# Kernel tuning notes

Measured on AMD Instinct MI355X. Metric: run time of the kernel, lower is better.

## Reference

```python
import jax, jax.numpy as jnp
import numpy as np

B, T, I, H, O = 512, 512, 128, 50, 10


def setup_inputs() -> dict:
    key = jax.random.key(0)
    ks = jax.random.split(key, 7)
    return {
        "x": jax.random.normal(ks[0], (B, T, I), dtype=jnp.float32),
        "W_ih": jax.random.normal(ks[1], (4 * H, I), dtype=jnp.float32) * 0.05,
        "W_hh": jax.random.normal(ks[2], (4 * H, H), dtype=jnp.float32) * 0.05,
        "b_ih": jax.random.normal(ks[3], (4 * H,), dtype=jnp.float32) * 0.05,
        "b_hh": jax.random.normal(ks[4], (4 * H,), dtype=jnp.float32) * 0.05,
        "W_fc": jax.random.normal(ks[5], (O, H), dtype=jnp.float32) * 0.05,
        "b_fc": jax.random.normal(ks[6], (O,), dtype=jnp.float32) * 0.05,
    }


def reference(x, W_ih, W_hh, b_ih, b_hh, W_fc, b_fc):
    # Single-layer LSTM (PyTorch gate order i,f,g,o), batch_first, zero init state.
    Bsz = x.shape[0]
    Hd = W_hh.shape[1]
    bias = b_ih + b_hh  # [4H]
    # Precompute input projections for all timesteps: [T, B, 4H]
    x_proj = jnp.einsum('bti,gi->tbg', x, W_ih) + bias

    def step(carry, xp_t):
        h, c = carry  # [B, H] each
        gates = xp_t + h @ W_hh.T  # [B, 4H]
        i, f, g, o = jnp.split(gates, 4, axis=-1)
        i = jax.nn.sigmoid(i)
        f = jax.nn.sigmoid(f)
        g = jnp.tanh(g)
        o = jax.nn.sigmoid(o)
        c = f * c + i * g
        h = o * jnp.tanh(c)
        return (h, c), None

    h0 = jnp.zeros((Bsz, Hd), dtype=x.dtype)
    c0 = jnp.zeros((Bsz, Hd), dtype=x.dtype)
    (h_last, _), _ = jax.lax.scan(step, (h0, c0), x_proj)
    return h_last @ W_fc.T + b_fc  # [B, O]
```

## Files before the change

### kernel.cpp

```cpp
#include <hip/hip_runtime.h>


#define BB 512
#define TT 512
#define II 128
#define HH 50
#define GG 200

typedef _Float16 half2v __attribute__((ext_vector_type(2)));
typedef _Float16 half8v __attribute__((ext_vector_type(8)));
typedef float float4v __attribute__((ext_vector_type(4)));

#if defined(__has_builtin)
#if __has_builtin(__builtin_amdgcn_fdot2)
#define HAVE_FDOT2 1
#endif
#if __has_builtin(__builtin_amdgcn_rcpf)
#define HAVE_RCPF 1
#endif
#endif

__device__ __forceinline__ float fdot2f(half2v a, half2v b, float c) {
#ifdef HAVE_FDOT2
    return __builtin_amdgcn_fdot2(a, b, c, false);
#else
    return c + (float)a[0] * (float)b[0] + (float)a[1] * (float)b[1];
#endif
}

__device__ __forceinline__ float frcp(float x) {
#ifdef HAVE_RCPF
    return __builtin_amdgcn_rcpf(x);
#else
    return 1.f / x;
#endif
}
__device__ __forceinline__ float fsig(float x) {
    return frcp(1.f + __expf(-x));
}
__device__ __forceinline__ float ftanh(float x) {
    return 2.f * fsig(2.f * x) - 1.f;
}

__global__ __launch_bounds__(256) void prep_kernel(
    const float* __restrict__ W_ih, const float* __restrict__ W_hh,
    const float* __restrict__ b_ih, const float* __restrict__ b_hh,
    _Float16* __restrict__ wfrags, _Float16* __restrict__ whh16,
    float* __restrict__ biasv)
{
    int idx = blockIdx.x * 256 + threadIdx.x;
    if (idx < 3328) {
        int lane = idx & 63, kc = (idx >> 6) & 3, nt = idx >> 8;
        int gp = nt * 16 + (lane & 15);
        int k0 = kc * 32 + ((lane >> 4) & 3) * 8;
        half8v v;
        if (gp < GG) {
            int u = gp >> 2, j = gp & 3;
            const float* wr = W_ih + (size_t)(j * HH + u) * II + k0;
            #pragma unroll
            for (int q = 0; q < 8; ++q) v[q] = (_Float16)wr[q];
        } else {
            #pragma unroll
            for (int q = 0; q < 8; ++q) v[q] = (_Float16)0.f;
        }
        *(half8v*)(wfrags + (size_t)idx * 8) = v;
    } else if (idx < 3328 + 2800) {
        int r = idx - 3328;
        int g = r / 14, j4 = r % 14;
        #pragma unroll
        for (int j = 0; j < 4; ++j) {
            int hidx = j4 * 4 + j;
            whh16[g * 56 + hidx] = (hidx < HH) ? (_Float16)W_hh[g * HH + hidx]
                                               : (_Float16)0.f;
        }
    } else if (idx < 3328 + 2800 + GG) {
        int gp = idx - 6128;
        int u = gp >> 2, j = gp & 3;
        biasv[gp] = b_ih[j * HH + u] + b_hh[j * HH + u];
    }
}

__global__
__attribute__((amdgpu_flat_work_group_size(256, 256)))
__attribute__((amdgpu_waves_per_eu(1, 2)))
void lstm_fused(
    const float* __restrict__ x, const _Float16* __restrict__ wfrags,
    const float* __restrict__ biasv, const _Float16* __restrict__ whh16,
    const float* __restrict__ W_fc, const float* __restrict__ b_fc,
    float* __restrict__ out)
{
    __shared__ __align__(16) _Float16 wflds[3328 * 8];
    __shared__ __align__(16) _Float16 xbuf[64 * GG];
    __shared__ float blds[GG];
    __shared__ __align__(16) _Float16 hbuf[2][56];
    __shared__ float hf32[HH];
    const int tid = threadIdx.x;
    const int b = blockIdx.x;
    const int w = tid >> 6, l = tid & 63;

    for (int s = tid; s < 3328; s += 256)
        *(float4v*)(wflds + (size_t)s * 8) = *(const float4v*)(wfrags + (size_t)s * 8);
    for (int s = tid; s < GG; s += 256) blds[s] = biasv[s];

    const int gp = (tid < GG) ? tid : 197;
    const int u = gp >> 2;
    const int gate = gp & 3;
    const int wrow = gate * HH + u;

    float4v wv[7];
    #pragma unroll
    for (int j = 0; j < 7; ++j)
        wv[j] = *(const float4v*)(whh16 + (size_t)wrow * 56 + j * 8);

    const int row = w * 16 + (l & 15);
    const int kq = (l >> 4) & 3;
    const float* xbase = x + ((size_t)b * TT + row) * II + kq * 8;

    float4 f0[4], f1[4];
    #pragma unroll
    for (int kc = 0; kc < 4; ++kc) {
        f0[kc] = *(const float4*)(xbase + kc * 32);
        f1[kc] = *(const float4*)(xbase + kc * 32 + 4);
    }

    if (tid < 56) {
        hbuf[0][tid] = (_Float16)0.f;
        hbuf[1][tid] = (_Float16)0.f;
    }
    float c = 0.f, hlast = 0.f;
    __syncthreads();

    const int colb = l & 15, rq = l >> 4;

    for (int ch = 0; ch < 8; ++ch) {
        half8v a[4];
        #pragma unroll
        for (int kc = 0; kc < 4; ++kc) {
            a[kc][0] = (_Float16)f0[kc].x; a[kc][1] = (_Float16)f0[kc].y;
            a[kc][2] = (_Float16)f0[kc].z; a[kc][3] = (_Float16)f0[kc].w;
            a[kc][4] = (_Float16)f1[kc].x; a[kc][5] = (_Float16)f1[kc].y;
            a[kc][6] = (_Float16)f1[kc].z; a[kc][7] = (_Float16)f1[kc].w;
        }
        if (ch + 1 < 8) {
            const float* xn = xbase + (size_t)(ch + 1) * 64 * II;
            #pragma unroll
            for (int kc = 0; kc < 4; ++kc) {
                f0[kc] = *(const float4*)(xn + kc * 32);
                f1[kc] = *(const float4*)(xn + kc * 32 + 4);
            }
        }

        float4v acc[13];
        #pragma unroll
        for (int nt = 0; nt < 13; ++nt) acc[nt] = (float4v){0.f, 0.f, 0.f, 0.f};
        #pragma unroll
        for (int kc = 0; kc < 4; ++kc) {
            #pragma unroll
            for (int nt = 0; nt < 13; ++nt) {
                half8v bf = *(const half8v*)(wflds + (size_t)(((nt * 4 + kc) * 64) + l) * 8);
                acc[nt] = __builtin_amdgcn_mfma_f32_16x16x32_f16(a[kc], bf, acc[nt], 0, 0, 0);
            }
        }
        #pragma unroll
        for (int nt = 0; nt < 13; ++nt) {
            int g = nt * 16 + colb;
            if (g < GG) {
                float bs = blds[g];
                #pragma unroll
                for (int reg = 0; reg < 4; ++reg)
                    xbuf[(w * 16 + rq * 4 + reg) * GG + g] = (_Float16)(acc[nt][reg] + bs);
            }
        }
        __syncthreads();

        #pragma unroll 4
        for (int t = 0; t < 64; ++t) {
            const int p = t & 1;
            float4v hv[7];
            #pragma unroll
            for (int j = 0; j < 7; ++j)
                hv[j] = *(const float4v*)(hbuf[p] + j * 8);

            float xpf = (float)xbuf[t * GG + gp];

            float a0 = 0.f, a1 = 0.f, a2 = 0.f, a3 = 0.f;
            #pragma unroll
            for (int j = 0; j < 7; ++j) {
                const half2v* hp = (const half2v*)&hv[j];
                const half2v* wp = (const half2v*)&wv[j];
                a0 = fdot2f(hp[0], wp[0], a0);
                a1 = fdot2f(hp[1], wp[1], a1);
                a2 = fdot2f(hp[2], wp[2], a2);
                a3 = fdot2f(hp[3], wp[3], a3);
            }
            float acg = ((a0 + a1) + (a2 + a3)) + xpf;

            bool isg = (gate == 2);
            float xin = isg ? 2.f * acg : acg;
            float sg = fsig(xin);
            float act = isg ? (2.f * sg - 1.f) : sg;

            int ai = __builtin_bit_cast(int, act);
            float gi = __builtin_bit_cast(float, __builtin_amdgcn_mov_dpp(ai, 0x00, 0xF, 0xF, true));
            float gf = __builtin_bit_cast(float, __builtin_amdgcn_mov_dpp(ai, 0x55, 0xF, 0xF, true));
            float gg = __builtin_bit_cast(float, __builtin_amdgcn_mov_dpp(ai, 0xAA, 0xF, 0xF, true));
            float go = __builtin_bit_cast(float, __builtin_amdgcn_mov_dpp(ai, 0xFF, 0xF, 0xF, true));

            c = gf * c + gi * gg;
            float hn = go * ftanh(c);

            if (tid < GG && gate == 0) hbuf[p ^ 1][u] = (_Float16)hn;
            __syncthreads();

            hlast = hn;
        }
    }

    if (tid < GG && gate == 0) hf32[u] = hlast;
    __syncthreads();
    if (tid < 10) {
        float a = b_fc[tid];
        #pragma unroll
        for (int kx = 0; kx < HH; ++kx)
            a += hf32[kx] * W_fc[tid * HH + kx];
        out[b * 10 + tid] = a;
    }
}

extern "C" void kernel_launch(void* const* d_in, const int* in_sizes, int n_in,
                              void* d_out, int out_size, void* d_ws, size_t ws_size,
                              hipStream_t stream)
{
    const float* x    = (const float*)d_in[0];
    const float* W_ih = (const float*)d_in[1];
    const float* W_hh = (const float*)d_in[2];
    const float* b_ih = (const float*)d_in[3];
    const float* b_hh = (const float*)d_in[4];
    const float* W_fc = (const float*)d_in[5];
    const float* b_fc = (const float*)d_in[6];
    float* out = (float*)d_out;
    char* wsb = (char*)d_ws;

    _Float16* wfrags = (_Float16*)wsb;
    _Float16* whh16  = (_Float16*)(wsb + 53248);
    float*    biasv  = (float*)(wsb + 53248 + 22400);

    prep_kernel<<<25, 256, 0, stream>>>(W_ih, W_hh, b_ih, b_hh,
                                        wfrags, whh16, biasv);
    lstm_fused<<<BB, 256, 0, stream>>>(x, wfrags, biasv, whh16,
                                       W_fc, b_fc, out);
}
```

Measured before the change: 349.1 us.

## Run LSTM recurrence in a single wave with bpermute hidden-state exchange

Each batch element now runs on one 64-lane wave instead of four. Each lane owns one hidden unit and computes all four of its gates, holding the four W_hh rows in registers. The hidden state is shared across lanes with DPP and ds_bpermute instead of an LDS buffer, which removes the per-timestep __syncthreads. The input projection is computed in 16-step chunks by the same wave with MFMA, so it is no longer spread over four waves. In exchange, each lane does four times more dot-product work per step, and the projection runs serially with the recurrence.

Result: slower. 367.6 us (+5.3%).

```diff
diff --git a/kernel.cpp b/kernel.cpp
--- a/kernel.cpp
+++ b/kernel.cpp
@@ -8,6 +8,7 @@
 #define GG 200
 
 typedef _Float16 half2v __attribute__((ext_vector_type(2)));
+typedef _Float16 half4v __attribute__((ext_vector_type(4)));
 typedef _Float16 half8v __attribute__((ext_vector_type(8)));
 typedef float float4v __attribute__((ext_vector_type(4)));
 
@@ -81,8 +82,8 @@
 }
 
 __global__
-__attribute__((amdgpu_flat_work_group_size(256, 256)))
-__attribute__((amdgpu_waves_per_eu(1, 2)))
+__attribute__((amdgpu_flat_work_group_size(64, 64)))
+__attribute__((amdgpu_waves_per_eu(1, 1)))
 void lstm_fused(
     const float* __restrict__ x, const _Float16* __restrict__ wfrags,
     const float* __restrict__ biasv, const _Float16* __restrict__ whh16,
@@ -90,31 +91,33 @@
     float* __restrict__ out)
 {
     __shared__ __align__(16) _Float16 wflds[3328 * 8];
-    __shared__ __align__(16) _Float16 xbuf[64 * GG];
-    __shared__ float blds[GG];
-    __shared__ __align__(16) _Float16 hbuf[2][56];
+    __shared__ __align__(16) _Float16 xbuf[16 * GG];
     __shared__ float hf32[HH];
-    const int tid = threadIdx.x;
+    const int l = threadIdx.x;
     const int b = blockIdx.x;
-    const int w = tid >> 6, l = tid & 63;
-
-    for (int s = tid; s < 3328; s += 256)
+    const int kk = (l < HH) ? l : (HH - 1);
+
+    for (int s = l; s < 3328; s += 64)
         *(float4v*)(wflds + (size_t)s * 8) = *(const float4v*)(wfrags + (size_t)s * 8);
-    for (int s = tid; s < GG; s += 256) blds[s] = biasv[s];
-
-    const int gp = (tid < GG) ? tid : 197;
-    const int u = gp >> 2;
-    const int gate = gp & 3;
-    const int wrow = gate * HH + u;
-
-    float4v wv[7];
+
+    float bs[13];
     #pragma unroll
-    for (int j = 0; j < 7; ++j)
-        wv[j] = *(const float4v*)(whh16 + (size_t)wrow * 56 + j * 8);
-
-    const int row = w * 16 + (l & 15);
-    const int kq = (l >> 4) & 3;
-    const float* xbase = x + ((size_t)b * TT + row) * II + kq * 8;
+    for (int nt = 0; nt < 13; ++nt) {
+        int g = nt * 16 + (l & 15);
+        bs[nt] = (g < GG) ? biasv[g] : 0.f;
+    }
+
+    float4v wr0[7], wr1[7], wr2[7], wr3[7];
+    #pragma unroll
+    for (int j = 0; j < 7; ++j) {
+        wr0[j] = *(const float4v*)(whh16 + (size_t)(kk      ) * 56 + j * 8);
+        wr1[j] = *(const float4v*)(whh16 + (size_t)(kk +  50) * 56 + j * 8);
+        wr2[j] = *(const float4v*)(whh16 + (size_t)(kk + 100) * 56 + j * 8);
+        wr3[j] = *(const float4v*)(whh16 + (size_t)(kk + 150) * 56 + j * 8);
+    }
+
+    const int rq = l >> 4;
+    const float* xbase = x + ((size_t)b * TT + (l & 15)) * II + rq * 8;
 
     float4 f0[4], f1[4];
     #pragma unroll
@@ -123,16 +126,10 @@
         f1[kc] = *(const float4*)(xbase + kc * 32 + 4);
     }
 
-    if (tid < 56) {
-        hbuf[0][tid] = (_Float16)0.f;
-        hbuf[1][tid] = (_Float16)0.f;
-    }
-    float c = 0.f, hlast = 0.f;
-    __syncthreads();
-
-    const int colb = l & 15, rq = l >> 4;
-
-    for (int ch = 0; ch < 8; ++ch) {
+    float c = 0.f, h = 0.f;
+    const int colb = l & 15;
+
+    for (int ch = 0; ch < 32; ++ch) {
         half8v a[4];
         #pragma unroll
         for (int kc = 0; kc < 4; ++kc) {
@@ -141,8 +138,8 @@
             a[kc][4] = (_Float16)f1[kc].x; a[kc][5] = (_Float16)f1[kc].y;
             a[kc][6] = (_Float16)f1[kc].z; a[kc][7] = (_Float16)f1[kc].w;
         }
-        if (ch + 1 < 8) {
-            const float* xn = xbase + (size_t)(ch + 1) * 64 * II;
+        if (ch + 1 < 32) {
+            const float* xn = xbase + (size_t)(ch + 1) * 16 * II;
             #pragma unroll
             for (int kc = 0; kc < 4; ++kc) {
                 f0[kc] = *(const float4*)(xn + kc * 32);
@@ -165,65 +162,59 @@
         for (int nt = 0; nt < 13; ++nt) {
             int g = nt * 16 + colb;
             if (g < GG) {
-                float bs = blds[g];
                 #pragma unroll
                 for (int reg = 0; reg < 4; ++reg)
-                    xbuf[(w * 16 + rq * 4 + reg) * GG + g] = (_Float16)(acc[nt][reg] + bs);
-            }
-        }
-        __syncthreads();
+                    xbuf[(rq * 4 + reg) * GG + g] = (_Float16)(acc[nt][reg] + bs[nt]);
+            }
+        }
 
         #pragma unroll 4
-        for (int t = 0; t < 64; ++t) {
-            const int p = t & 1;
-            float4v hv[7];
-            #pragma unroll
-            for (int j = 0; j < 7; ++j)
-                hv[j] = *(const float4v*)(hbuf[p] + j * 8);
-
-            float xpf = (float)xbuf[t * GG + gp];
-
-            float a0 = 0.f, a1 = 0.f, a2 = 0.f, a3 = 0.f;
-            #pragma unroll
-            for (int j = 0; j < 7; ++j) {
-                const half2v* hp = (const half2v*)&hv[j];
-                const half2v* wp = (const half2v*)&wv[j];
-                a0 = fdot2f(hp[0], wp[0], a0);
-                a1 = fdot2f(hp[1], wp[1], a1);
-                a2 = fdot2f(hp[2], wp[2], a2);
-                a3 = fdot2f(hp[3], wp[3], a3);
-            }
-            float acg = ((a0 + a1) + (a2 + a3)) + xpf;
-
-            bool isg = (gate == 2);
-            float xin = isg ? 2.f * acg : acg;
-            float sg = fsig(xin);
-            float act = isg ? (2.f * sg - 1.f) : sg;
-
-            int ai = __builtin_bit_cast(int, act);
-            float gi = __builtin_bit_cast(float, __builtin_amdgcn_mov_dpp(ai, 0x00, 0xF, 0xF, true));
-            float gf = __builtin_bit_cast(float, __builtin_amdgcn_mov_dpp(ai, 0x55, 0xF, 0xF, true));
-            float gg = __builtin_bit_cast(float, __builtin_amdgcn_mov_dpp(ai, 0xAA, 0xF, 0xF, true));
-            float go = __builtin_bit_cast(float, __builtin_amdgcn_mov_dpp(ai, 0xFF, 0xF, 0xF, true));
-
-            c = gf * c + gi * gg;
-            float hn = go * ftanh(c);
-
-            if (tid < GG && gate == 0) hbuf[p ^ 1][u] = (_Float16)hn;
-            __syncthreads();
-
-            hlast = hn;
-        }
-    }
-
-    if (tid < GG && gate == 0) hf32[u] = hlast;
-    __syncthreads();
-    if (tid < 10) {
-        float a = b_fc[tid];
+        for (int t = 0; t < 16; ++t) {
+            half4v p = *(const half4v*)(xbuf + t * GG + kk * 4);
+            float aI0 = (float)p[0];
+            float aF0 = (float)p[1];
+            float aG0 = (float)p[2];
+            float aO0 = (float)p[3];
+            float aI1 = 0.f, aF1 = 0.f, aG1 = 0.f, aO1 = 0.f;
+
+            _Float16 h16 = (_Float16)h;
+            int hi = (int)__builtin_bit_cast(unsigned short, h16);
+            int hsw = __builtin_amdgcn_mov_dpp(hi, 0xB1, 0xF, 0xF, true);
+            int pk = hi | (hsw << 16);
+
+            #pragma unroll
+            for (int m = 0; m < 25; ++m) {
+                int sp = __builtin_amdgcn_ds_bpermute(8 * m, pk);
+                half2v hq = __builtin_bit_cast(half2v, sp);
+                int j = m >> 2, q = m & 3;
+                if (m & 1) {
+                    aI1 = fdot2f(hq, ((const half2v*)&wr0[j])[q], aI1);
+                    aF1 = fdot2f(hq, ((const half2v*)&wr1[j])[q], aF1);
+                    aG1 = fdot2f(hq, ((const half2v*)&wr2[j])[q], aG1);
+                    aO1 = fdot2f(hq, ((const half2v*)&wr3[j])[q], aO1);
+                } else {
+                    aI0 = fdot2f(hq, ((const half2v*)&wr0[j])[q], aI0);
+                    aF0 = fdot2f(hq, ((const half2v*)&wr1[j])[q], aF0);
+                    aG0 = fdot2f(hq, ((const half2v*)&wr2[j])[q], aG0);
+                    aO0 = fdot2f(hq, ((const half2v*)&wr3[j])[q], aO0);
+                }
+            }
+            float ii = fsig(aI0 + aI1);
+            float ff = fsig(aF0 + aF1);
+            float gg = ftanh(aG0 + aG1);
+            float oo = fsig(aO0 + aO1);
+            c = ff * c + ii * gg;
+            h = oo * ftanh(c);
+        }
+    }
+
+    if (l < HH) hf32[l] = h;
+    if (l < 10) {
+        float a = b_fc[l];
         #pragma unroll
         for (int kx = 0; kx < HH; ++kx)
-            a += hf32[kx] * W_fc[tid * HH + kx];
-        out[b * 10 + tid] = a;
+            a += hf32[kx] * W_fc[l * HH + kx];
+        out[b * 10 + l] = a;
     }
 }
 
@@ -247,6 +238,6 @@
 
     prep_kernel<<<25, 256, 0, stream>>>(W_ih, W_hh, b_ih, b_hh,
                                         wfrags, whh16, biasv);
-    lstm_fused<<<BB, 256, 0, stream>>>(x, wfrags, biasv, whh16,
-                                       W_fc, b_fc, out);
-}
+    lstm_fused<<<BB, 64, 0, stream>>>(x, wfrags, biasv, whh16,
+                                      W_fc, b_fc, out);
+}
```
